# Optimization experiments

Hardware: AMD Instinct MI355X
Metric: run time of the kernel (lower is better)

Reference implementation:

```python
import jax, jax.numpy as jnp
import numpy as np

INPUT_DIM = 512
PROJ_DIM = 128
HIDDEN = INPUT_DIM // 2  # 256


def setup_inputs() -> dict:
    key = jax.random.key(0)
    ks = jax.random.split(key, 6)
    B = 8192
    s1 = 1.0 / np.sqrt(INPUT_DIM)
    s2 = 1.0 / np.sqrt(HIDDEN)
    return {
        "fused_text": jax.random.normal(ks[0], (B, INPUT_DIM), dtype=jnp.float32),
        "x": jax.random.normal(ks[1], (B, INPUT_DIM), dtype=jnp.float32),
        # generator layer 1: Linear(input_dim, input_dim//2), torch layout [out, in]
        "W1": jax.random.uniform(ks[2], (HIDDEN, INPUT_DIM), jnp.float32, -s1, s1),
        "b1": jax.random.uniform(ks[3], (HIDDEN,), jnp.float32, -s1, s1),
        # generator layer 2: Linear(input_dim//2, proj_dim * input_dim)
        "W2": jax.random.uniform(ks[4], (PROJ_DIM * INPUT_DIM, HIDDEN), jnp.float32, -s2, s2),
        "b2": jax.random.uniform(ks[5], (PROJ_DIM * INPUT_DIM,), jnp.float32, -s2, s2),
    }


def reference(fused_text, x, W1, b1, W2, b2):
    B = fused_text.shape[0]
    # hypernetwork generator MLP
    h = jax.nn.relu(fused_text @ W1.T + b1)          # [B, hidden]
    w_flat = h @ W2.T + b2                           # [B, proj_dim * input_dim]
    W = w_flat.reshape(B, PROJ_DIM, INPUT_DIM)       # per-sample weights
    # per-sample projection: bmm(W, x[..., None]).squeeze(-1)
    out = jnp.einsum("bpi,bi->bp", W, x)             # [B, proj_dim]
    return out
```

## Files before the change

### kernel.cpp

```cpp
#include <hip/hip_runtime.h>
#include <stdint.h>

#define B_SZ   8192
#define IN_DIM 512
#define HID    256
#define PROJ   128

typedef __attribute__((ext_vector_type(8))) short bf16x8;
typedef __attribute__((ext_vector_type(4))) float f32x4;

#define GLDS16(gp, lp) __builtin_amdgcn_global_load_lds( \
    (const __attribute__((address_space(1))) void*)(gp), \
    (__attribute__((address_space(3))) void*)(lp), 16, 0, 0)

__device__ __forceinline__ unsigned short f2bf(float f) {
    union { float f; uint32_t u; } c; c.f = f;
    uint32_t u = c.u;
    uint32_t r = (u + 0x7fffu + ((u >> 16) & 1u)) >> 16;
    return (unsigned short)r;
}
__device__ __forceinline__ float bfhi(uint32_t v) {
    union { uint32_t u; float f; } c; c.u = v & 0xffff0000u; return c.f;
}
__device__ __forceinline__ float bflo(uint32_t v) {
    union { uint32_t u; float f; } c; c.u = v << 16; return c.f;
}

__global__ __launch_bounds__(256) void k0_prep(
        const float4* __restrict__ W2, ushort4* __restrict__ W2b,
        const float* __restrict__ x, unsigned short* __restrict__ xTb) {
    __shared__ float tile[64][65];
    const int bid = blockIdx.x;
    if (bid < 2048) {
        const int nW2 = (PROJ * IN_DIM * HID) / 4;
        const int stride = 2048 * 256;
        for (int i = bid * 256 + threadIdx.x; i < nW2; i += stride) {
            float4 v = W2[i];
            ushort4 o;
            o.x = f2bf(v.x); o.y = f2bf(v.y); o.z = f2bf(v.z); o.w = f2bf(v.w);
            W2b[i] = o;
        }
    } else {
        const int tb = bid - 2048;
        const int bi = tb & 7, bb = tb >> 3;
        const int i0 = bi * 64, b0 = bb * 64;
        const int t = threadIdx.x;
        const int c = t & 63, r4 = t >> 6;
        #pragma unroll
        for (int rr = 0; rr < 64; rr += 4)
            tile[rr + r4][c] = x[(size_t)(b0 + rr + r4) * IN_DIM + i0 + c];
        __syncthreads();
        #pragma unroll
        for (int rr = 0; rr < 64; rr += 4)
            xTb[(size_t)(i0 + rr + r4) * B_SZ + b0 + c] = f2bf(tile[c][rr + r4]);
    }
}

__device__ __forceinline__ bf16x8 ld_cvt8(const float* __restrict__ s) {
    float4 a = *(const float4*)s;
    float4 b = *(const float4*)(s + 4);
    bf16x8 r;
    r[0] = (short)f2bf(a.x); r[1] = (short)f2bf(a.y);
    r[2] = (short)f2bf(a.z); r[3] = (short)f2bf(a.w);
    r[4] = (short)f2bf(b.x); r[5] = (short)f2bf(b.y);
    r[6] = (short)f2bf(b.z); r[7] = (short)f2bf(b.w);
    return r;
}

__global__ __launch_bounds__(256) void k1_hidden(
        const float* __restrict__ ft,
        const float* __restrict__ W1,
        const float* __restrict__ b1,
        unsigned short* __restrict__ hb) {
    const int lane = threadIdx.x & 63;
    const int wv   = threadIdx.x >> 6;
    const int l15  = lane & 15, q = lane >> 4;
    const int b0 = blockIdx.x * 64;
    const int n0 = wv * 64;

    f32x4 acc[4][4];
    const f32x4 z4 = {0.f, 0.f, 0.f, 0.f};
    #pragma unroll
    for (int mt = 0; mt < 4; ++mt)
        #pragma unroll
        for (int nt = 0; nt < 4; ++nt) acc[mt][nt] = z4;

    for (int kq = 0; kq < 16; ++kq) {
        const int koff = kq * 32 + q * 8;
        bf16x8 a[4], bb[4];
        #pragma unroll
        for (int mt = 0; mt < 4; ++mt)
            a[mt] = ld_cvt8(ft + (size_t)(b0 + mt*16 + l15) * IN_DIM + koff);
        #pragma unroll
        for (int nt = 0; nt < 4; ++nt)
            bb[nt] = ld_cvt8(W1 + (size_t)(n0 + nt*16 + l15) * IN_DIM + koff);
        #pragma unroll
        for (int mt = 0; mt < 4; ++mt)
            #pragma unroll
            for (int nt = 0; nt < 4; ++nt)
                acc[mt][nt] = __builtin_amdgcn_mfma_f32_16x16x32_bf16(
                    a[mt], bb[nt], acc[mt][nt], 0, 0, 0);
    }
    #pragma unroll
    for (int nt = 0; nt < 4; ++nt) {
        float bias = b1[n0 + nt*16 + l15];
        #pragma unroll
        for (int mt = 0; mt < 4; ++mt)
            #pragma unroll
            for (int r = 0; r < 4; ++r) {
                float v = acc[mt][nt][r] + bias;
                v = fmaxf(v, 0.f);
                hb[(size_t)(b0 + mt*16 + q*4 + r) * HID + n0 + nt*16 + l15] = f2bf(v);
            }
    }
}

__global__ __launch_bounds__(256, 4) void k3_main(
        const unsigned short* __restrict__ W2b,
        const unsigned short* __restrict__ hb,
        const unsigned short* __restrict__ xTb,
        const float* __restrict__ b2,
        float* __restrict__ out) {
    __shared__ unsigned short lbs[2][64 * 128];
    const int tid  = threadIdx.x;
    const int lane = tid & 63;
    const int wv   = tid >> 6;
    const int l15  = lane & 15, q = lane >> 4;
    const int pgrp = blockIdx.x & 63;
    const int bsup = blockIdx.x >> 6;
    const int p0   = pgrp * 2;
    const int b0w  = bsup * 128 + wv * 32;
    const f32x4 z4 = {0.f, 0.f, 0.f, 0.f};

    const int grow_sub = lane >> 4;
    const int cbase    = (lane & 15) ^ grow_sub;

    const int qx   = q ^ (l15 & 3);
    const int kbit = (l15 >> 2) & 1;

    float oacc[2][2][4];
    #pragma unroll
    for (int pp = 0; pp < 2; ++pp)
        #pragma unroll
        for (int mt = 0; mt < 2; ++mt)
            #pragma unroll
            for (int r = 0; r < 4; ++r) oacc[pp][mt][r] = 0.f;

    bf16x8 afr[2][4];

    {
        #pragma unroll
        for (int jj = 0; jj < 4; ++jj) {
            const int j   = wv * 4 + jj;
            const int row = j * 4 + grow_sub;
            const int p   = row >> 5, ir = row & 31;
            const int c   = cbase ^ (4 * (jj & 1));
            const unsigned short* g = W2b
                + ((size_t)(p0 + p) * IN_DIM + ir) * HID + c * 8;
            GLDS16(g, &lbs[0][j * 512]);
        }
    }

    #pragma unroll 1
    for (int t = 0; t < 32; ++t) {
        __syncthreads();

        if (t < 31) {
            const int tn = t + 1;
            const int kh = tn >> 4, i0 = (tn & 15) * 32;
            unsigned short* Ld = lbs[tn & 1];
            #pragma unroll
            for (int jj = 0; jj < 4; ++jj) {
                const int j   = wv * 4 + jj;
                const int row = j * 4 + grow_sub;
                const int p   = row >> 5, ir = row & 31;
                const int c   = cbase ^ (4 * (jj & 1));
                const unsigned short* g = W2b
                    + ((size_t)(p0 + p) * IN_DIM + i0 + ir) * HID + kh * 128 + c * 8;
                GLDS16(g, &Ld[j * 512]);
            }
        }

        const int kh = t >> 4;
        if ((t & 15) == 0) {
            #pragma unroll
            for (int mt = 0; mt < 2; ++mt) {
                const unsigned short* hrow =
                    hb + (size_t)(b0w + mt*16 + l15) * HID + kh * 128 + q * 8;
                #pragma unroll
                for (int kq = 0; kq < 4; ++kq)
                    afr[mt][kq] = *(const bf16x8*)(hrow + kq * 32);
            }
        }

        const unsigned short* Lb = lbs[t & 1];
        const int i0 = (t & 15) * 32;

        #pragma unroll
        for (int sub = 0; sub < 2; ++sub) {
            const int irow = i0 + sub * 16 + l15;
            uint2 xv[2];
            const unsigned short* xp = xTb + (size_t)irow * B_SZ + b0w + q * 4;
            #pragma unroll
            for (int mt = 0; mt < 2; ++mt)
                xv[mt] = *(const uint2*)(xp + mt * 16);

            const float b2v = (kh == 0) ? b2[p0 * 512 + irow] : 0.f;
            const float b2w = (kh == 0) ? b2[(p0 + 1) * 512 + irow] : 0.f;

            #pragma unroll
            for (int pp = 0; pp < 2; ++pp) {
                const unsigned short* Bp = Lb + (pp*32 + sub*16 + l15) * 128;
                bf16x8 bfr[4];
                #pragma unroll
                for (int kq = 0; kq < 4; ++kq) {
                    const int cpos = qx + 4 * (kq ^ kbit);
                    bfr[kq] = *(const bf16x8*)(Bp + cpos * 8);
                }

                f32x4 D[2];
                #pragma unroll
                for (int mt = 0; mt < 2; ++mt)
                    D[mt] = __builtin_amdgcn_mfma_f32_16x16x32_bf16(afr[mt][0], bfr[0], z4, 0, 0, 0);
                #pragma unroll
                for (int kq = 1; kq < 4; ++kq)
                    #pragma unroll
                    for (int mt = 0; mt < 2; ++mt)
                        D[mt] = __builtin_amdgcn_mfma_f32_16x16x32_bf16(afr[mt][kq], bfr[kq], D[mt], 0, 0, 0);

                const float bb = pp ? b2w : b2v;
                #pragma unroll
                for (int mt = 0; mt < 2; ++mt) {
                    oacc[pp][mt][0] = fmaf(D[mt][0] + bb, bflo(xv[mt].x), oacc[pp][mt][0]);
                    oacc[pp][mt][1] = fmaf(D[mt][1] + bb, bfhi(xv[mt].x), oacc[pp][mt][1]);
                    oacc[pp][mt][2] = fmaf(D[mt][2] + bb, bflo(xv[mt].y), oacc[pp][mt][2]);
                    oacc[pp][mt][3] = fmaf(D[mt][3] + bb, bfhi(xv[mt].y), oacc[pp][mt][3]);
                }
            }
        }
    }

    #pragma unroll
    for (int pp = 0; pp < 2; ++pp)
        #pragma unroll
        for (int mt = 0; mt < 2; ++mt)
            #pragma unroll
            for (int r = 0; r < 4; ++r) {
                float v = oacc[pp][mt][r];
                v += __shfl_xor(v, 1, 16);
                v += __shfl_xor(v, 2, 16);
                v += __shfl_xor(v, 4, 16);
                v += __shfl_xor(v, 8, 16);
                if (l15 == 0)
                    out[(size_t)(b0w + mt*16 + q*4 + r) * PROJ + p0 + pp] = v;
            }
}

extern "C" void kernel_launch(void* const* d_in, const int* in_sizes, int n_in,
                              void* d_out, int out_size, void* d_ws, size_t ws_size,
                              hipStream_t stream) {
    const float* ft = (const float*)d_in[0];
    const float* x  = (const float*)d_in[1];
    const float* W1 = (const float*)d_in[2];
    const float* b1 = (const float*)d_in[3];
    const float* W2 = (const float*)d_in[4];
    const float* b2 = (const float*)d_in[5];
    float* out = (float*)d_out;

    char* ws = (char*)d_ws;
    unsigned short* W2b = (unsigned short*)(ws);
    unsigned short* hb  = (unsigned short*)(ws + 33554432);
    unsigned short* xTb = (unsigned short*)(ws + 37748736);

    hipLaunchKernelGGL(k0_prep, dim3(3072), dim3(256), 0, stream,
        (const float4*)W2, (ushort4*)W2b, x, xTb);
    hipLaunchKernelGGL(k1_hidden, dim3(128), dim3(256), 0, stream, ft, W1, b1, hb);
    hipLaunchKernelGGL(k3_main, dim3(4096), dim3(256), 0, stream, W2b, hb, xTb, b2, out);
}
```

Baseline: 489.6 us.

## Double batch tile per block in k3_main and use lane-major LDS layout

Each wave now covers 64 batch rows instead of 32, so the grid halves and every W2 tile staged in LDS is reused across twice as many samples, cutting global/L2 traffic for W2. The LDS layout becomes lane-major: each wave loads its own 16-row slice so that B-fragment reads index straight by lane, which removes the XOR swizzle arithmetic. The price is more accumulator and A-fragment registers (occupancy hint drops from 4 to 3) and fewer blocks to spread across CUs.

```diff
diff --git a/kernel.cpp b/kernel.cpp
--- a/kernel.cpp
+++ b/kernel.cpp
@@ -115,13 +115,13 @@
     }
 }
 
-__global__ __launch_bounds__(256, 4) void k3_main(
+__global__ __launch_bounds__(256, 3) void k3_main(
         const unsigned short* __restrict__ W2b,
         const unsigned short* __restrict__ hb,
         const unsigned short* __restrict__ xTb,
         const float* __restrict__ b2,
         float* __restrict__ out) {
-    __shared__ unsigned short lbs[2][64 * 128];
+    __shared__ unsigned short lbs[2][8192];
     const int tid  = threadIdx.x;
     const int lane = tid & 63;
     const int wv   = tid >> 6;
@@ -129,36 +129,27 @@
     const int pgrp = blockIdx.x & 63;
     const int bsup = blockIdx.x >> 6;
     const int p0   = pgrp * 2;
-    const int b0w  = bsup * 128 + wv * 32;
+    const int b0w  = bsup * 256 + wv * 64;
     const f32x4 z4 = {0.f, 0.f, 0.f, 0.f};
 
-    const int grow_sub = lane >> 4;
-    const int cbase    = (lane & 15) ^ grow_sub;
-
-    const int qx   = q ^ (l15 & 3);
-    const int kbit = (l15 >> 2) & 1;
-
-    float oacc[2][2][4];
+    const unsigned short* wrowbase =
+        W2b + ((size_t)(p0 + (wv >> 1)) * IN_DIM + (wv & 1) * 16 + l15) * HID + q * 8;
+
+    float oacc[2][4][4];
     #pragma unroll
     for (int pp = 0; pp < 2; ++pp)
         #pragma unroll
-        for (int mt = 0; mt < 2; ++mt)
+        for (int mt = 0; mt < 4; ++mt)
             #pragma unroll
             for (int r = 0; r < 4; ++r) oacc[pp][mt][r] = 0.f;
 
-    bf16x8 afr[2][4];
+    bf16x8 afr[4][4];
 
     {
-        #pragma unroll
-        for (int jj = 0; jj < 4; ++jj) {
-            const int j   = wv * 4 + jj;
-            const int row = j * 4 + grow_sub;
-            const int p   = row >> 5, ir = row & 31;
-            const int c   = cbase ^ (4 * (jj & 1));
-            const unsigned short* g = W2b
-                + ((size_t)(p0 + p) * IN_DIM + ir) * HID + c * 8;
-            GLDS16(g, &lbs[0][j * 512]);
-        }
+        unsigned short* Ld = &lbs[0][wv * 2048];
+        #pragma unroll
+        for (int jj = 0; jj < 4; ++jj)
+            GLDS16(wrowbase + jj * 32, Ld + jj * 512);
     }
 
     #pragma unroll 1
@@ -167,24 +158,18 @@
 
         if (t < 31) {
             const int tn = t + 1;
-            const int kh = tn >> 4, i0 = (tn & 15) * 32;
-            unsigned short* Ld = lbs[tn & 1];
-            #pragma unroll
-            for (int jj = 0; jj < 4; ++jj) {
-                const int j   = wv * 4 + jj;
-                const int row = j * 4 + grow_sub;
-                const int p   = row >> 5, ir = row & 31;
-                const int c   = cbase ^ (4 * (jj & 1));
-                const unsigned short* g = W2b
-                    + ((size_t)(p0 + p) * IN_DIM + i0 + ir) * HID + kh * 128 + c * 8;
-                GLDS16(g, &Ld[j * 512]);
-            }
+            const int kh_n = tn >> 4, i0_n = (tn & 15) * 32;
+            unsigned short* Ld = &lbs[tn & 1][wv * 2048];
+            const unsigned short* gs = wrowbase + (size_t)i0_n * HID + kh_n * 128;
+            #pragma unroll
+            for (int jj = 0; jj < 4; ++jj)
+                GLDS16(gs + jj * 32, Ld + jj * 512);
         }
 
         const int kh = t >> 4;
         if ((t & 15) == 0) {
             #pragma unroll
-            for (int mt = 0; mt < 2; ++mt) {
+            for (int mt = 0; mt < 4; ++mt) {
                 const unsigned short* hrow =
                     hb + (size_t)(b0w + mt*16 + l15) * HID + kh * 128 + q * 8;
                 #pragma unroll
@@ -193,44 +178,44 @@
             }
         }
 
-        const unsigned short* Lb = lbs[t & 1];
+        const unsigned short* Lb = &lbs[t & 1][lane * 8];
         const int i0 = (t & 15) * 32;
 
         #pragma unroll
         for (int sub = 0; sub < 2; ++sub) {
             const int irow = i0 + sub * 16 + l15;
-            uint2 xv[2];
+            uint2 xv[4];
             const unsigned short* xp = xTb + (size_t)irow * B_SZ + b0w + q * 4;
             #pragma unroll
-            for (int mt = 0; mt < 2; ++mt)
+            for (int mt = 0; mt < 4; ++mt)
                 xv[mt] = *(const uint2*)(xp + mt * 16);
 
-            const float b2v = (kh == 0) ? b2[p0 * 512 + irow] : 0.f;
-            const float b2w = (kh == 0) ? b2[(p0 + 1) * 512 + irow] : 0.f;
+            float b2v = 0.f, b2w = 0.f;
+            if (kh == 0) {
+                b2v = b2[p0 * 512 + irow];
+                b2w = b2[(p0 + 1) * 512 + irow];
+            }
 
             #pragma unroll
             for (int pp = 0; pp < 2; ++pp) {
-                const unsigned short* Bp = Lb + (pp*32 + sub*16 + l15) * 128;
                 bf16x8 bfr[4];
                 #pragma unroll
-                for (int kq = 0; kq < 4; ++kq) {
-                    const int cpos = qx + 4 * (kq ^ kbit);
-                    bfr[kq] = *(const bf16x8*)(Bp + cpos * 8);
-                }
-
-                f32x4 D[2];
-                #pragma unroll
-                for (int mt = 0; mt < 2; ++mt)
+                for (int kq = 0; kq < 4; ++kq)
+                    bfr[kq] = *(const bf16x8*)(Lb + ((pp*2 + sub)*4 + kq) * 512);
+
+                f32x4 D[4];
+                #pragma unroll
+                for (int mt = 0; mt < 4; ++mt)
                     D[mt] = __builtin_amdgcn_mfma_f32_16x16x32_bf16(afr[mt][0], bfr[0], z4, 0, 0, 0);
                 #pragma unroll
                 for (int kq = 1; kq < 4; ++kq)
                     #pragma unroll
-                    for (int mt = 0; mt < 2; ++mt)
+                    for (int mt = 0; mt < 4; ++mt)
                         D[mt] = __builtin_amdgcn_mfma_f32_16x16x32_bf16(afr[mt][kq], bfr[kq], D[mt], 0, 0, 0);
 
                 const float bb = pp ? b2w : b2v;
                 #pragma unroll
-                for (int mt = 0; mt < 2; ++mt) {
+                for (int mt = 0; mt < 4; ++mt) {
                     oacc[pp][mt][0] = fmaf(D[mt][0] + bb, bflo(xv[mt].x), oacc[pp][mt][0]);
                     oacc[pp][mt][1] = fmaf(D[mt][1] + bb, bfhi(xv[mt].x), oacc[pp][mt][1]);
                     oacc[pp][mt][2] = fmaf(D[mt][2] + bb, bflo(xv[mt].y), oacc[pp][mt][2]);
@@ -243,7 +228,7 @@
     #pragma unroll
     for (int pp = 0; pp < 2; ++pp)
         #pragma unroll
-        for (int mt = 0; mt < 2; ++mt)
+        for (int mt = 0; mt < 4; ++mt)
             #pragma unroll
             for (int r = 0; r < 4; ++r) {
                 float v = oacc[pp][mt][r];
@@ -275,5 +260,5 @@
     hipLaunchKernelGGL(k0_prep, dim3(3072), dim3(256), 0, stream,
         (const float4*)W2, (ushort4*)W2b, x, xTb);
     hipLaunchKernelGGL(k1_hidden, dim3(128), dim3(256), 0, stream, ft, W1, b1, hb);
-    hipLaunchKernelGGL(k3_main, dim3(4096), dim3(256), 0, stream, W2b, hb, xTb, b2, out);
-}
+    hipLaunchKernelGGL(k3_main, dim3(2048), dim3(256), 0, stream, W2b, hb, xTb, b2, out);
+}
```

After: 551.3 us. 1.13x slower.
